# Performance work log

Measured on AMD Instinct MI355X. Metric: run time of the kernel, lower is better.

## Reference

```python
import jax, jax.numpy as jnp
import numpy as np

MEAN = jnp.array([0.485, 0.456, 0.406], dtype=jnp.float32).reshape(3, 1, 1)
STD = jnp.array([0.229, 0.224, 0.225], dtype=jnp.float32).reshape(3, 1, 1)
BLOCK = 8  # JPEG DCT block size


def _conv2(x, k):
    # x: [B,H,W], k: [kh,kw] -> SAME conv per image
    kern = k[None, None].astype(x.dtype)
    y = jax.lax.conv_general_dilated(x[:, None], kern, (1, 1), 'SAME')
    return y[:, 0]


def _box3(x):
    return _conv2(x, jnp.ones((3, 3), jnp.float32) / 9.0)


def _normalize(f):
    # per-image min-max to [0,1]; zero map if degenerate (matches _normalize)
    fmin = f.min(axis=(-2, -1), keepdims=True)
    fmax = f.max(axis=(-2, -1), keepdims=True)
    rng = fmax - fmin
    safe = jnp.where(rng < 1e-8, 1.0, rng)
    return jnp.where(rng < 1e-8, 0.0, (f - fmin) / safe)


def _forward(x):
    # denormalize ImageNet stats, clamp, scale to [0,255] (continuous; uint8 round omitted)
    img = jnp.clip(x * STD + MEAN, 0.0, 1.0) * 255.0  # [B,3,H,W]
    gray = 0.299 * img[:, 0] + 0.587 * img[:, 1] + 0.114 * img[:, 2]  # [B,H,W]

    # --- channel 0: spectral residual anomaly (FFT) ---
    F = jnp.fft.fft2(gray)
    logmag = jnp.log(jnp.abs(F) + 1e-8)
    resid = logmag - _box3(logmag)            # high-freq log-spectrum residual
    phase = jnp.angle(F)
    sal = jnp.abs(jnp.fft.ifft2(jnp.exp(resid) * jnp.exp(1j * phase))) ** 2
    M_spec = _normalize(sal)

    # --- channel 1: resampling artifact (2nd-derivative / Laplacian magnitude) ---
    lap_k = jnp.array([[0., 1., 0.], [1., -4., 1.], [0., 1., 0.]], jnp.float32)
    M_resamp = _normalize(jnp.abs(_conv2(gray, lap_k)))

    # --- channel 2: JPEG blockiness (gradient energy on 8x8 block boundaries) ---
    B, H, W = gray.shape
    dh = jnp.abs(gray - jnp.roll(gray, 1, axis=-1))  # horizontal neighbor diff
    dv = jnp.abs(gray - jnp.roll(gray, 1, axis=-2))  # vertical neighbor diff
    col_mask = (jnp.arange(W) % BLOCK == 0).astype(gray.dtype)  # [W]
    row_mask = (jnp.arange(H) % BLOCK == 0).astype(gray.dtype)  # [H]
    blockiness = dh * col_mask[None, None, :] + dv * row_mask[None, :, None]
    M_jpeg = _normalize(blockiness)

    return jnp.stack([M_spec, M_resamp, M_jpeg], axis=1)  # [B,3,H,W]


def setup_inputs() -> dict:
    key = jax.random.key(0)
    x = jax.random.normal(key, (16, 3, 512, 512), dtype=jnp.float32)
    return {"x": x}


def reference(x):
    return _forward(x)
```

## Files before the change

kernel.cpp:

```cpp
#include <hip/hip_runtime.h>
#include <hip/hip_bf16.h>
#include <math.h>

#define W 512
#define H 512
#define HW 262144
#define NB 16

__device__ __forceinline__ int brev9(int x) { return (int)(__brev((unsigned)x) >> 23); }
__device__ __forceinline__ int pad17(int i) { return i + (i >> 4); }

__device__ __forceinline__ void block_minmax_atomic(float vmin, float vmax,
                                                    unsigned* minU, unsigned* maxU) {
  #pragma unroll
  for (int o = 32; o; o >>= 1) {
    vmin = fminf(vmin, __shfl_xor(vmin, o));
    vmax = fmaxf(vmax, __shfl_xor(vmax, o));
  }
  __shared__ float smin[4], smax[4];
  int wid = threadIdx.x >> 6;
  int lane = threadIdx.x & 63;
  if (lane == 0) { smin[wid] = vmin; smax[wid] = vmax; }
  __syncthreads();
  if (threadIdx.x == 0) {
    int nw = (blockDim.x + 63) >> 6;
    float m = smin[0], M = smax[0];
    for (int i = 1; i < nw; ++i) { m = fminf(m, smin[i]); M = fmaxf(M, smax[i]); }
    atomicMin(minU, __float_as_uint(m));
    atomicMax(maxU, __float_as_uint(M));
  }
  __syncthreads();
}

__global__ void k_init(unsigned* mm) {
  int t = threadIdx.x;
  if (t < 48) mm[t] = 0x7F800000u;
  else if (t < 96) mm[t] = 0u;
}

__device__ __forceinline__ float gray_one(float r, float g, float b) {
  float R = fminf(fmaxf(fmaf(r, 0.229f, 0.485f), 0.f), 1.f) * 255.f;
  float G = fminf(fmaxf(fmaf(g, 0.224f, 0.456f), 0.f), 1.f) * 255.f;
  float B = fminf(fmaxf(fmaf(b, 0.225f, 0.406f), 0.f), 1.f) * 255.f;
  return fmaf(0.299f, R, fmaf(0.587f, G, 0.114f * B));
}

__device__ __forceinline__ void tw_init(float2* tw, int t, int nthr) {
  for (int k = t; k < 256; k += nthr) {
    float sn, cs;
    __sincosf(-6.283185307179586f * (float)k * (1.f / 512.f), &sn, &cs);
    tw[k] = make_float2(cs, sn);
  }
}

#define QUAD_BODY(LOADA0, LOADA1, LOADA2, LOADA3)                                   \
  float e0r = sre[LOADA0], e0i = sim[LOADA0];                                       \
  float e1r = sre[LOADA1], e1i = sim[LOADA1];                                       \
  float e2r = sre[LOADA2], e2i = sim[LOADA2];                                       \
  float e3r = sre[LOADA3], e3i = sim[LOADA3];                                       \
  float t1r = fmaf(e1r, w1c, -e1i * w1s), t1i = fmaf(e1r, w1s, e1i * w1c);          \
  float t3r = fmaf(e3r, w1c, -e3i * w1s), t3i = fmaf(e3r, w1s, e3i * w1c);          \
  float A0r = e0r + t1r, A0i = e0i + t1i;                                           \
  float A1r = e0r - t1r, A1i = e0i - t1i;                                           \
  float A2r = e2r + t3r, A2i = e2i + t3i;                                           \
  float A3r = e2r - t3r, A3i = e2i - t3i;                                           \
  float t2r = fmaf(A2r, w2c, -A2i * w2s), t2i = fmaf(A2r, w2s, A2i * w2c);          \
  float t4r = fmaf(A3r, w3c, -A3i * w3s), t4i = fmaf(A3r, w3s, A3i * w3c);          \
  sre[LOADA0] = A0r + t2r; sim[LOADA0] = A0i + t2i;                                 \
  sre[LOADA2] = A0r - t2r; sim[LOADA2] = A0i - t2i;                                 \
  sre[LOADA1] = A1r + t4r; sim[LOADA1] = A1i + t4i;                                 \
  sre[LOADA3] = A1r - t4r; sim[LOADA3] = A1i - t4i;

template <int DIR>
__device__ __forceinline__ void fft512_q(float* sre, float* sim, const float2* tw, int t) {
  #pragma unroll
  for (int sp = 1; sp <= 7; sp += 2) {
    __syncthreads();
    int h = 1 << (sp - 1);
    int j = t & (h - 1);
    int q = ((t >> (sp - 1)) << (sp + 1)) + j;
    float2 w1t = tw[j << (9 - sp)];
    float2 w2t = tw[j << (8 - sp)];
    float2 w3t = tw[(j + h) << (8 - sp)];
    float w1c = w1t.x, w1s = (DIR > 0) ? w1t.y : -w1t.y;
    float w2c = w2t.x, w2s = (DIR > 0) ? w2t.y : -w2t.y;
    float w3c = w3t.x, w3s = (DIR > 0) ? w3t.y : -w3t.y;
    int a0 = pad17(q), a1 = pad17(q + h), a2 = pad17(q + 2 * h), a3 = pad17(q + 3 * h);
    QUAD_BODY(a0, a1, a2, a3)
  }
  __syncthreads();
  #pragma unroll
  for (int bb = 0; bb < 2; ++bb) {
    int bf = t + (bb << 7);
    float2 w = tw[bf];
    float cs = w.x, sn = (DIR > 0) ? w.y : -w.y;
    int a0 = pad17(bf), a1 = pad17(bf + 256);
    float ur = sre[a0], ui = sim[a0];
    float vr = sre[a1], vi = sim[a1];
    float tr = fmaf(vr, cs, -vi * sn);
    float ti = fmaf(vr, sn, vi * cs);
    sre[a0] = ur + tr; sim[a0] = ui + ti;
    sre[a1] = ur - tr; sim[a1] = ui - ti;
  }
  __syncthreads();
}

template <int DIR>
__device__ __forceinline__ void fft512x8_q(float* sre, float* sim, const float2* tw,
                                           int c, int tc) {
  #pragma unroll
  for (int sp = 1; sp <= 7; sp += 2) {
    __syncthreads();
    int h = 1 << (sp - 1);
    #pragma unroll
    for (int m = 0; m < 4; ++m) {
      int qq = tc + (m << 5);
      int j = qq & (h - 1);
      int q = ((qq >> (sp - 1)) << (sp + 1)) + j;
      float2 w1t = tw[j << (9 - sp)];
      float2 w2t = tw[j << (8 - sp)];
      float2 w3t = tw[(j + h) << (8 - sp)];
      float w1c = w1t.x, w1s = (DIR > 0) ? w1t.y : -w1t.y;
      float w2c = w2t.x, w2s = (DIR > 0) ? w2t.y : -w2t.y;
      float w3c = w3t.x, w3s = (DIR > 0) ? w3t.y : -w3t.y;
      int a0 = q * 9 + c, a1 = (q + h) * 9 + c, a2 = (q + 2 * h) * 9 + c, a3 = (q + 3 * h) * 9 + c;
      QUAD_BODY(a0, a1, a2, a3)
    }
  }
  __syncthreads();
  #pragma unroll
  for (int bb = 0; bb < 8; ++bb) {
    int bf = tc + (bb << 5);
    float2 w = tw[bf];
    float cs = w.x, sn = (DIR > 0) ? w.y : -w.y;
    int a0 = bf * 9 + c, a1 = (bf + 256) * 9 + c;
    float ur = sre[a0], ui = sim[a0];
    float vr = sre[a1], vi = sim[a1];
    float tr = fmaf(vr, cs, -vi * sn);
    float ti = fmaf(vr, sn, vi * cs);
    sre[a0] = ur + tr; sim[a0] = ui + ti;
    sre[a1] = ur - tr; sim[a1] = ui - ti;
  }
  __syncthreads();
}

__global__ void k_rowfft(const float* __restrict__ x, float* __restrict__ gray,
                         float2* __restrict__ C) {
  int r = blockIdx.x, b = blockIdx.y, t = threadIdx.x;
  __shared__ float sre[544], sim[544];
  __shared__ float2 tw[256];
  tw_init(tw, t, 128);
  const float* xr = x + (((size_t)(b * 3 + 0)) << 18) + r * W;
  const float* xg = x + (((size_t)(b * 3 + 1)) << 18) + r * W;
  const float* xb = x + (((size_t)(b * 3 + 2)) << 18) + r * W;
  float* gr = gray + (((size_t)b) << 18) + r * W;
  #pragma unroll
  for (int k = t; k < 512; k += 128) {
    float g = gray_one(xr[k], xg[k], xb[k]);
    gr[k] = g;
    int kr = pad17(brev9(k));
    sre[kr] = g; sim[kr] = 0.f;
  }
  fft512_q<1>(sre, sim, tw, t);
  float2* Crow = C + (((size_t)b) << 18) + r * W;
  #pragma unroll
  for (int k = t; k < 512; k += 128) {
    int kp = pad17(k);
    Crow[k] = make_float2(sre[kp], sim[kp]);
  }
}

__global__ void k_ch12(const float* __restrict__ gray, float* __restrict__ out, unsigned* mm) {
  int slab = blockIdx.x, b = blockIdx.y, t = threadIdx.x;
  const float* gb = gray + (((size_t)b) << 18);
  float* o1 = out + (((size_t)(b * 3 + 1)) << 18);
  float* o2 = out + (((size_t)(b * 3 + 2)) << 18);
  float mn1 = INFINITY, mx1 = -INFINITY, mn2 = INFINITY, mx2 = -INFINITY;
  for (int i4 = t; i4 < 32 * 128; i4 += 256) {
    int r = (slab << 5) + (i4 >> 7);
    int k4 = (i4 & 127) << 2;
    const float* row = gb + r * W;
    float4 c4 = *(const float4*)(row + k4);
    float s_lfw = row[(k4 + W - 1) & (W - 1)];
    float s_rt  = (k4 < W - 4) ? row[k4 + 4] : 0.f;
    float4 up4 = (r > 0)     ? *(const float4*)(gb + (r - 1) * W + k4) : make_float4(0.f, 0.f, 0.f, 0.f);
    float4 dn4 = (r < H - 1) ? *(const float4*)(gb + (r + 1) * W + k4) : make_float4(0.f, 0.f, 0.f, 0.f);
    float c[4]  = {c4.x, c4.y, c4.z, c4.w};
    float up[4] = {up4.x, up4.y, up4.z, up4.w};
    float dn[4] = {dn4.x, dn4.y, dn4.z, dn4.w};
    float lap[4], blk[4];
    #pragma unroll
    for (int e = 0; e < 4; ++e) {
      float lf = (e == 0) ? ((k4 > 0) ? s_lfw : 0.f) : c[e - 1];
      float rt = (e == 3) ? s_rt : c[e + 1];
      lap[e] = fabsf(lf + rt + up[e] + dn[e] - 4.f * c[e]);
      mn1 = fminf(mn1, lap[e]); mx1 = fmaxf(mx1, lap[e]);
    }
    bool rowb = ((r & 7) == 0);
    float pv[4] = {0.f, 0.f, 0.f, 0.f};
    if (rowb) {
      int rp = (r + H - 1) & (H - 1);
      float4 p4 = *(const float4*)(gb + rp * W + k4);
      pv[0] = p4.x; pv[1] = p4.y; pv[2] = p4.z; pv[3] = p4.w;
    }
    #pragma unroll
    for (int e = 0; e < 4; ++e) {
      float v = 0.f;
      if (e == 0 && ((k4 & 7) == 0)) v += fabsf(c[0] - s_lfw);
      if (rowb) v += fabsf(c[e] - pv[e]);
      blk[e] = v;
      mn2 = fminf(mn2, v); mx2 = fmaxf(mx2, v);
    }
    *(float4*)(o1 + r * W + k4) = make_float4(lap[0], lap[1], lap[2], lap[3]);
    *(float4*)(o2 + r * W + k4) = make_float4(blk[0], blk[1], blk[2], blk[3]);
  }
  block_minmax_atomic(mn1, mx1, mm + (b * 3 + 1), mm + 48 + (b * 3 + 1));
  block_minmax_atomic(mn2, mx2, mm + (b * 3 + 2), mm + 48 + (b * 3 + 2));
}

__global__ void k_colfft_fwd(float2* __restrict__ C, float* __restrict__ L) {
  int b = blockIdx.y, col0 = blockIdx.x << 3, t = threadIdx.x;
  __shared__ float sre[512 * 9], sim[512 * 9];
  __shared__ float2 tw[256];
  tw_init(tw, t, 256);
  float2* Cb = C + (((size_t)b) << 18);
  int c = t & 7, q = t >> 3;
  #pragma unroll
  for (int it = 0; it < 16; ++it) {
    int r = (it << 5) + q;
    float2 v = Cb[r * W + col0 + c];
    int rr = brev9(r);
    sre[rr * 9 + c] = v.x; sim[rr * 9 + c] = v.y;
  }
  fft512x8_q<1>(sre, sim, tw, t >> 5, t & 31);
  float* Lb = L + (((size_t)b) << 18);
  #pragma unroll
  for (int it = 0; it < 16; ++it) {
    int r = (it << 5) + q;
    float re = sre[r * 9 + c], im = sim[r * 9 + c];
    Cb[r * W + col0 + c] = make_float2(re, im);
    Lb[r * W + col0 + c] = logf(sqrtf(fmaf(re, re, im * im)) + 1e-8f);
  }
}

__global__ void k_rowifft_g(float2* __restrict__ C, const float* __restrict__ L) {
  int r = blockIdx.x, b = blockIdx.y, t = threadIdx.x;
  __shared__ float sre[544], sim[544], l0[512], lm[512], lp[512];
  __shared__ float2 tw[256];
  tw_init(tw, t, 128);
  const float* Lb = L + (((size_t)b) << 18);
  #pragma unroll
  for (int k = t; k < 512; k += 128) {
    l0[k] = Lb[r * W + k];
    lm[k] = (r > 0) ? Lb[(r - 1) * W + k] : 0.f;
    lp[k] = (r < H - 1) ? Lb[(r + 1) * W + k] : 0.f;
  }
  __syncthreads();
  float2* Crow = C + (((size_t)b) << 18) + r * W;
  #pragma unroll
  for (int k = t; k < 512; k += 128) {
    float sum = lm[k] + l0[k] + lp[k];
    if (k > 0)     sum += lm[k - 1] + l0[k - 1] + lp[k - 1];
    if (k < W - 1) sum += lm[k + 1] + l0[k + 1] + lp[k + 1];
    float resid = l0[k] - sum * (1.f / 9.f);
    float2 cv = Crow[k];
    float mag = sqrtf(fmaf(cv.x, cv.x, cv.y * cv.y));
    float er = __expf(resid);
    float gr, gi;
    if (mag > 1e-30f) { float tt = er / mag; gr = cv.x * tt; gi = cv.y * tt; }
    else { gr = er; gi = 0.f; }
    int kr = pad17(brev9(k));
    sre[kr] = gr; sim[kr] = gi;
  }
  fft512_q<-1>(sre, sim, tw, t);
  #pragma unroll
  for (int k = t; k < 512; k += 128) {
    int kp = pad17(k);
    Crow[k] = make_float2(sre[kp] * (1.f / 512.f), sim[kp] * (1.f / 512.f));
  }
}

__global__ void k_colifft_sal(const float2* __restrict__ C, float* __restrict__ out, unsigned* mm) {
  int b = blockIdx.y, col0 = blockIdx.x << 3, t = threadIdx.x;
  __shared__ float sre[512 * 9], sim[512 * 9];
  __shared__ float2 tw[256];
  tw_init(tw, t, 256);
  const float2* Cb = C + (((size_t)b) << 18);
  int c = t & 7, q = t >> 3;
  #pragma unroll
  for (int it = 0; it < 16; ++it) {
    int r = (it << 5) + q;
    float2 v = Cb[r * W + col0 + c];
    int rr = brev9(r);
    sre[rr * 9 + c] = v.x; sim[rr * 9 + c] = v.y;
  }
  fft512x8_q<-1>(sre, sim, tw, t >> 5, t & 31);
  float* ob = out + (((size_t)(b * 3 + 0)) << 18);
  float mn = INFINITY, mx = -INFINITY;
  #pragma unroll
  for (int it = 0; it < 16; ++it) {
    int r = (it << 5) + q;
    float re = sre[r * 9 + c], im = sim[r * 9 + c];
    float sal = fmaf(re, re, im * im) * 3.814697265625e-6f;
    ob[r * W + col0 + c] = sal;
    mn = fminf(mn, sal); mx = fmaxf(mx, sal);
  }
  block_minmax_atomic(mn, mx, mm + b * 3, mm + 48 + b * 3);
}

__global__ void k_norm(float* __restrict__ out, const unsigned* __restrict__ mm) {
  int i = blockIdx.x * blockDim.x + threadIdx.x;
  size_t base = ((size_t)i) << 2;
  int map = (int)(base >> 18);
  float mn = __uint_as_float(mm[map]);
  float mx = __uint_as_float(mm[48 + map]);
  float rng = mx - mn;
  float4 v = *(float4*)(out + base);
  float4 o;
  if (rng < 1e-8f) {
    o = make_float4(0.f, 0.f, 0.f, 0.f);
  } else {
    float inv = 1.f / rng;
    o.x = (v.x - mn) * inv;
    o.y = (v.y - mn) * inv;
    o.z = (v.z - mn) * inv;
    o.w = (v.w - mn) * inv;
  }
  *(float4*)(out + base) = o;
}

extern "C" void kernel_launch(void* const* d_in, const int* in_sizes, int n_in,
                              void* d_out, int out_size, void* d_ws, size_t ws_size,
                              hipStream_t stream) {
  const float* x = (const float*)d_in[0];
  float* out = (float*)d_out;

  float* gray = (float*)d_ws;
  float2* C = (float2*)((char*)d_ws + (size_t)NB * HW * sizeof(float));
  float* L = (float*)((char*)C + (size_t)NB * HW * sizeof(float2));
  unsigned* mm = (unsigned*)((char*)L + (size_t)NB * HW * sizeof(float));

  k_init<<<1, 96, 0, stream>>>(mm);
  k_rowfft<<<dim3(H, NB), 128, 0, stream>>>(x, gray, C);
  k_ch12<<<dim3(16, NB), 256, 0, stream>>>(gray, out, mm);
  k_colfft_fwd<<<dim3(W / 8, NB), 256, 0, stream>>>(C, L);
  k_rowifft_g<<<dim3(H, NB), 128, 0, stream>>>(C, L);
  k_colifft_sal<<<dim3(W / 8, NB), 256, 0, stream>>>(C, out, mm);
  k_norm<<<12288, 256, 0, stream>>>(out, mm);
}
```

Before: 226.7 us.

## Fuse pipeline into one persistent cooperative kernel with grid syncs

Replaces the seven-kernel launch sequence with one persistent cooperative kernel that runs every stage in turn, separated by grid-wide syncs: row FFT, Laplacian/blockiness maps, column FFT with log-magnitude, row inverse FFT, column inverse FFT with saliency, then min/max reduction and normalization. Per-block atomic min/max is replaced by per-slab partial min/max arrays reduced in a dedicated stage, and the ch1/ch2 work now runs in smaller 8-row slabs interleaved with the column FFT phase. The aim is to remove launch gaps and the init kernel. The cost is several grid barriers, and occupancy is limited by the shared-memory footprint and launch_bounds. If the cooperative launch fails, it falls back to the old launches.

New measurement: 548.4 us. 2.42x slower.

```diff
diff --git a/kernel.cpp b/kernel.cpp
--- a/kernel.cpp
+++ b/kernel.cpp
@@ -1,56 +1,23 @@
 #include <hip/hip_runtime.h>
-#include <hip/hip_bf16.h>
+#include <hip/hip_cooperative_groups.h>
 #include <math.h>
+
+namespace cg = cooperative_groups;
 
 #define W 512
 #define H 512
 #define HW 262144
 #define NB 16
+#define TPB 256
 
 __device__ __forceinline__ int brev9(int x) { return (int)(__brev((unsigned)x) >> 23); }
 __device__ __forceinline__ int pad17(int i) { return i + (i >> 4); }
-
-__device__ __forceinline__ void block_minmax_atomic(float vmin, float vmax,
-                                                    unsigned* minU, unsigned* maxU) {
-  #pragma unroll
-  for (int o = 32; o; o >>= 1) {
-    vmin = fminf(vmin, __shfl_xor(vmin, o));
-    vmax = fmaxf(vmax, __shfl_xor(vmax, o));
-  }
-  __shared__ float smin[4], smax[4];
-  int wid = threadIdx.x >> 6;
-  int lane = threadIdx.x & 63;
-  if (lane == 0) { smin[wid] = vmin; smax[wid] = vmax; }
-  __syncthreads();
-  if (threadIdx.x == 0) {
-    int nw = (blockDim.x + 63) >> 6;
-    float m = smin[0], M = smax[0];
-    for (int i = 1; i < nw; ++i) { m = fminf(m, smin[i]); M = fmaxf(M, smax[i]); }
-    atomicMin(minU, __float_as_uint(m));
-    atomicMax(maxU, __float_as_uint(M));
-  }
-  __syncthreads();
-}
-
-__global__ void k_init(unsigned* mm) {
-  int t = threadIdx.x;
-  if (t < 48) mm[t] = 0x7F800000u;
-  else if (t < 96) mm[t] = 0u;
-}
 
 __device__ __forceinline__ float gray_one(float r, float g, float b) {
   float R = fminf(fmaxf(fmaf(r, 0.229f, 0.485f), 0.f), 1.f) * 255.f;
   float G = fminf(fmaxf(fmaf(g, 0.224f, 0.456f), 0.f), 1.f) * 255.f;
   float B = fminf(fmaxf(fmaf(b, 0.225f, 0.406f), 0.f), 1.f) * 255.f;
   return fmaf(0.299f, R, fmaf(0.587f, G, 0.114f * B));
-}
-
-__device__ __forceinline__ void tw_init(float2* tw, int t, int nthr) {
-  for (int k = t; k < 256; k += nthr) {
-    float sn, cs;
-    __sincosf(-6.283185307179586f * (float)k * (1.f / 512.f), &sn, &cs);
-    tw[k] = make_float2(cs, sn);
-  }
 }
 
 #define QUAD_BODY(LOADA0, LOADA1, LOADA2, LOADA3)                                   \
@@ -142,6 +109,288 @@
     sre[a1] = ur - tr; sim[a1] = ui - ti;
   }
   __syncthreads();
+}
+
+
+__device__ __forceinline__ void block_minmax_store(float vmin, float vmax,
+                                                   float* dmn, float* dmx,
+                                                   float* s_mn, float* s_mx) {
+  #pragma unroll
+  for (int o = 32; o; o >>= 1) {
+    vmin = fminf(vmin, __shfl_xor(vmin, o));
+    vmax = fmaxf(vmax, __shfl_xor(vmax, o));
+  }
+  int wid = threadIdx.x >> 6, lane = threadIdx.x & 63;
+  if (lane == 0) { s_mn[wid] = vmin; s_mx[wid] = vmax; }
+  __syncthreads();
+  if (threadIdx.x == 0) {
+    *dmn = fminf(fminf(s_mn[0], s_mn[1]), fminf(s_mn[2], s_mn[3]));
+    *dmx = fmaxf(fmaxf(s_mx[0], s_mx[1]), fmaxf(s_mx[2], s_mx[3]));
+  }
+  __syncthreads();
+}
+
+__global__ __launch_bounds__(TPB, 4) void k_mega(
+    const float* __restrict__ x, float* gray, float2* C, float* L,
+    float* mm, float* pmn, float* pmx, float* out) {
+  cg::grid_group gg = cg::this_grid();
+  __shared__ float smem[9216];
+  __shared__ float2 tw[256];
+  __shared__ float s_mn[4], s_mx[4];
+  const int g = blockIdx.x, t = threadIdx.x, nblk = gridDim.x;
+
+  {
+    float sn, cs;
+    __sincosf(-6.283185307179586f * (float)t * (1.f / 512.f), &sn, &cs);
+    tw[t] = make_float2(cs, sn);
+  }
+
+  {
+    const int sub = t >> 7, tt = t & 127;
+    float* sre = smem + sub * 1088;
+    float* sim = sre + 544;
+    for (int p = g; p < 4096; p += nblk) {
+      int R = (p << 1) + sub;
+      int b = R >> 9, r = R & 511;
+      const float* xr = x + (((size_t)(b * 3 + 0)) << 18) + r * W;
+      const float* xg = x + (((size_t)(b * 3 + 1)) << 18) + r * W;
+      const float* xb = x + (((size_t)(b * 3 + 2)) << 18) + r * W;
+      float* gr = gray + (((size_t)b) << 18) + r * W;
+      #pragma unroll
+      for (int k = tt; k < 512; k += 128) {
+        float gv = gray_one(xr[k], xg[k], xb[k]);
+        gr[k] = gv;
+        int kr = pad17(brev9(k));
+        sre[kr] = gv; sim[kr] = 0.f;
+      }
+      fft512_q<1>(sre, sim, tw, tt);
+      float2* Crow = C + (((size_t)b) << 18) + r * W;
+      #pragma unroll
+      for (int k = tt; k < 512; k += 128) {
+        int kp = pad17(k);
+        Crow[k] = make_float2(sre[kp], sim[kp]);
+      }
+      __syncthreads();
+    }
+  }
+  gg.sync();
+
+  for (int u2 = g; u2 < 1024; u2 += nblk) {
+    const int b = u2 >> 6, slab = u2 & 63, r0 = slab << 3;
+    const float* gb = gray + (((size_t)b) << 18);
+    float* o1 = out + (((size_t)(b * 3 + 1)) << 18);
+    float* o2 = out + (((size_t)(b * 3 + 2)) << 18);
+    float mn1 = INFINITY, mx1 = -INFINITY, mn2 = INFINITY, mx2 = -INFINITY;
+    for (int u = t; u < 8 * 128; u += TPB) {
+      int r = r0 + (u >> 7);
+      int k4 = (u & 127) << 2;
+      const float* row = gb + r * W;
+      float4 c4 = *(const float4*)(row + k4);
+      float s_lfw = row[(k4 + W - 1) & (W - 1)];
+      float s_rt  = (k4 < W - 4) ? row[k4 + 4] : 0.f;
+      float4 up4 = (r > 0)     ? *(const float4*)(gb + (r - 1) * W + k4) : make_float4(0.f, 0.f, 0.f, 0.f);
+      float4 dn4 = (r < H - 1) ? *(const float4*)(gb + (r + 1) * W + k4) : make_float4(0.f, 0.f, 0.f, 0.f);
+      float c[4]  = {c4.x, c4.y, c4.z, c4.w};
+      float up[4] = {up4.x, up4.y, up4.z, up4.w};
+      float dn[4] = {dn4.x, dn4.y, dn4.z, dn4.w};
+      float lap[4], blk[4];
+      #pragma unroll
+      for (int e = 0; e < 4; ++e) {
+        float lf = (e == 0) ? ((k4 > 0) ? s_lfw : 0.f) : c[e - 1];
+        float rt = (e == 3) ? s_rt : c[e + 1];
+        lap[e] = fabsf(lf + rt + up[e] + dn[e] - 4.f * c[e]);
+        mn1 = fminf(mn1, lap[e]); mx1 = fmaxf(mx1, lap[e]);
+      }
+      bool rowb = ((r & 7) == 0);
+      float pv[4] = {0.f, 0.f, 0.f, 0.f};
+      if (rowb) {
+        int rp = (r + H - 1) & (H - 1);
+        float4 p4 = *(const float4*)(gb + rp * W + k4);
+        pv[0] = p4.x; pv[1] = p4.y; pv[2] = p4.z; pv[3] = p4.w;
+      }
+      #pragma unroll
+      for (int e = 0; e < 4; ++e) {
+        float v = 0.f;
+        if (e == 0 && ((k4 & 7) == 0)) v += fabsf(c[0] - s_lfw);
+        if (rowb) v += fabsf(c[e] - pv[e]);
+        blk[e] = v;
+        mn2 = fminf(mn2, v); mx2 = fmaxf(mx2, v);
+      }
+      *(float4*)(o1 + r * W + k4) = make_float4(lap[0], lap[1], lap[2], lap[3]);
+      *(float4*)(o2 + r * W + k4) = make_float4(blk[0], blk[1], blk[2], blk[3]);
+    }
+    block_minmax_store(mn1, mx1, &pmn[(b * 3 + 1) * 64 + slab], &pmx[(b * 3 + 1) * 64 + slab], s_mn, s_mx);
+    block_minmax_store(mn2, mx2, &pmn[(b * 3 + 2) * 64 + slab], &pmx[(b * 3 + 2) * 64 + slab], s_mn, s_mx);
+  }
+
+  for (int u2 = g; u2 < 1024; u2 += nblk) {
+    const int b = u2 >> 6, col0 = (u2 & 63) << 3;
+    float* sre = smem;
+    float* sim = smem + 4608;
+    float2* Cb = C + (((size_t)b) << 18);
+    int c = t & 7, q = t >> 3;
+    __syncthreads();
+    #pragma unroll
+    for (int it = 0; it < 16; ++it) {
+      int r = (it << 5) + q;
+      float2 v = Cb[r * W + col0 + c];
+      int rr = brev9(r);
+      sre[rr * 9 + c] = v.x; sim[rr * 9 + c] = v.y;
+    }
+    fft512x8_q<1>(sre, sim, tw, t >> 5, t & 31);
+    float* Lb = L + (((size_t)b) << 18);
+    #pragma unroll
+    for (int it = 0; it < 16; ++it) {
+      int r = (it << 5) + q;
+      float re = sre[r * 9 + c], im = sim[r * 9 + c];
+      Cb[r * W + col0 + c] = make_float2(re, im);
+      Lb[r * W + col0 + c] = logf(sqrtf(fmaf(re, re, im * im)) + 1e-8f);
+    }
+  }
+  gg.sync();
+
+  {
+    const int sub = t >> 7, tt = t & 127;
+    float* sre = smem + sub * 1088;
+    float* sim = sre + 544;
+    float* l0 = smem + 2176 + sub * 1536;
+    float* lm = l0 + 512;
+    float* lp = l0 + 1024;
+    for (int p = g; p < 4096; p += nblk) {
+      int R = (p << 1) + sub;
+      int b = R >> 9, r = R & 511;
+      const float* Lb = L + (((size_t)b) << 18);
+      #pragma unroll
+      for (int k = tt; k < 512; k += 128) {
+        l0[k] = Lb[r * W + k];
+        lm[k] = (r > 0) ? Lb[(r - 1) * W + k] : 0.f;
+        lp[k] = (r < H - 1) ? Lb[(r + 1) * W + k] : 0.f;
+      }
+      __syncthreads();
+      float2* Crow = C + (((size_t)b) << 18) + r * W;
+      #pragma unroll
+      for (int k = tt; k < 512; k += 128) {
+        float sum = lm[k] + l0[k] + lp[k];
+        if (k > 0)     sum += lm[k - 1] + l0[k - 1] + lp[k - 1];
+        if (k < W - 1) sum += lm[k + 1] + l0[k + 1] + lp[k + 1];
+        float resid = l0[k] - sum * (1.f / 9.f);
+        float2 cv = Crow[k];
+        float mag = sqrtf(fmaf(cv.x, cv.x, cv.y * cv.y));
+        float er = __expf(resid);
+        float gr2, gi;
+        if (mag > 1e-30f) { float tt2 = er / mag; gr2 = cv.x * tt2; gi = cv.y * tt2; }
+        else { gr2 = er; gi = 0.f; }
+        int kr = pad17(brev9(k));
+        sre[kr] = gr2; sim[kr] = gi;
+      }
+      fft512_q<-1>(sre, sim, tw, tt);
+      #pragma unroll
+      for (int k = tt; k < 512; k += 128) {
+        int kp = pad17(k);
+        Crow[k] = make_float2(sre[kp] * (1.f / 512.f), sim[kp] * (1.f / 512.f));
+      }
+      __syncthreads();
+    }
+  }
+  gg.sync();
+
+  for (int u2 = g; u2 < 1024; u2 += nblk) {
+    const int b = u2 >> 6, slab = u2 & 63, col0 = slab << 3;
+    float* sre = smem;
+    float* sim = smem + 4608;
+    const float2* Cb = C + (((size_t)b) << 18);
+    int c = t & 7, q = t >> 3;
+    __syncthreads();
+    #pragma unroll
+    for (int it = 0; it < 16; ++it) {
+      int r = (it << 5) + q;
+      float2 v = Cb[r * W + col0 + c];
+      int rr = brev9(r);
+      sre[rr * 9 + c] = v.x; sim[rr * 9 + c] = v.y;
+    }
+    fft512x8_q<-1>(sre, sim, tw, t >> 5, t & 31);
+    float* ob = out + (((size_t)(b * 3 + 0)) << 18);
+    float mn = INFINITY, mx = -INFINITY;
+    #pragma unroll
+    for (int it = 0; it < 16; ++it) {
+      int r = (it << 5) + q;
+      float re = sre[r * 9 + c], im = sim[r * 9 + c];
+      float sal = fmaf(re, re, im * im) * 3.814697265625e-6f;
+      ob[r * W + col0 + c] = sal;
+      mn = fminf(mn, sal); mx = fmaxf(mx, sal);
+    }
+    block_minmax_store(mn, mx, &pmn[(b * 3 + 0) * 64 + slab], &pmx[(b * 3 + 0) * 64 + slab], s_mn, s_mx);
+  }
+  gg.sync();
+
+  for (int m = g; m < 48; m += nblk) {
+    if (t < 64) {
+      float vmn = pmn[m * 64 + t];
+      float vmx = pmx[m * 64 + t];
+      #pragma unroll
+      for (int o = 32; o; o >>= 1) {
+        vmn = fminf(vmn, __shfl_xor(vmn, o));
+        vmx = fmaxf(vmx, __shfl_xor(vmx, o));
+      }
+      if (t == 0) { mm[m] = vmn; mm[48 + m] = vmx; }
+    }
+  }
+  gg.sync();
+
+  for (int idx = g * TPB + t; idx < 3145728; idx += nblk * TPB) {
+    int map = idx >> 16;
+    float mn = mm[map], mx = mm[48 + map];
+    float rng = mx - mn;
+    float4 v = *(float4*)(out + ((size_t)idx << 2));
+    float4 o;
+    if (rng < 1e-8f) {
+      o = make_float4(0.f, 0.f, 0.f, 0.f);
+    } else {
+      float inv = 1.f / rng;
+      o.x = (v.x - mn) * inv;
+      o.y = (v.y - mn) * inv;
+      o.z = (v.z - mn) * inv;
+      o.w = (v.w - mn) * inv;
+    }
+    *(float4*)(out + ((size_t)idx << 2)) = o;
+  }
+}
+
+
+__device__ __forceinline__ void block_minmax_atomic(float vmin, float vmax,
+                                                    unsigned* minU, unsigned* maxU) {
+  #pragma unroll
+  for (int o = 32; o; o >>= 1) {
+    vmin = fminf(vmin, __shfl_xor(vmin, o));
+    vmax = fmaxf(vmax, __shfl_xor(vmax, o));
+  }
+  __shared__ float smin[4], smax[4];
+  int wid = threadIdx.x >> 6;
+  int lane = threadIdx.x & 63;
+  if (lane == 0) { smin[wid] = vmin; smax[wid] = vmax; }
+  __syncthreads();
+  if (threadIdx.x == 0) {
+    int nw = (blockDim.x + 63) >> 6;
+    float m = smin[0], M = smax[0];
+    for (int i = 1; i < nw; ++i) { m = fminf(m, smin[i]); M = fmaxf(M, smax[i]); }
+    atomicMin(minU, __float_as_uint(m));
+    atomicMax(maxU, __float_as_uint(M));
+  }
+  __syncthreads();
+}
+
+__global__ void k_init(unsigned* mm) {
+  int t = threadIdx.x;
+  if (t < 48) mm[t] = 0x7F800000u;
+  else if (t < 96) mm[t] = 0u;
+}
+
+__device__ __forceinline__ void tw_init(float2* tw, int t, int nthr) {
+  for (int k = t; k < 256; k += nthr) {
+    float sn, cs;
+    __sincosf(-6.283185307179586f * (float)k * (1.f / 512.f), &sn, &cs);
+    tw[k] = make_float2(cs, sn);
+  }
 }
 
 __global__ void k_rowfft(const float* __restrict__ x, float* __restrict__ gray,
@@ -338,13 +587,35 @@
   float* gray = (float*)d_ws;
   float2* C = (float2*)((char*)d_ws + (size_t)NB * HW * sizeof(float));
   float* L = (float*)((char*)C + (size_t)NB * HW * sizeof(float2));
-  unsigned* mm = (unsigned*)((char*)L + (size_t)NB * HW * sizeof(float));
-
-  k_init<<<1, 96, 0, stream>>>(mm);
-  k_rowfft<<<dim3(H, NB), 128, 0, stream>>>(x, gray, C);
-  k_ch12<<<dim3(16, NB), 256, 0, stream>>>(gray, out, mm);
-  k_colfft_fwd<<<dim3(W / 8, NB), 256, 0, stream>>>(C, L);
-  k_rowifft_g<<<dim3(H, NB), 128, 0, stream>>>(C, L);
-  k_colifft_sal<<<dim3(W / 8, NB), 256, 0, stream>>>(C, out, mm);
-  k_norm<<<12288, 256, 0, stream>>>(out, mm);
-}
+  void* mmv = (void*)((char*)L + (size_t)NB * HW * sizeof(float));
+
+  bool done = false;
+  int occ = 0;
+  hipError_t qe = hipOccupancyMaxActiveBlocksPerMultiprocessor(&occ, k_mega, TPB, 0);
+  if (qe == hipSuccess && occ > 0) {
+    int nblk = occ * 256;
+    if (nblk > 2048) nblk = 2048;
+    float* mmf = (float*)mmv;
+    float* pmn = mmf + 96;
+    float* pmx = pmn + 48 * 64;
+    void* args[] = {(void*)&x, (void*)&gray, (void*)&C, (void*)&L,
+                    (void*)&mmf, (void*)&pmn, (void*)&pmx, (void*)&out};
+    hipError_t le = hipLaunchCooperativeKernel((const void*)k_mega, dim3(nblk),
+                                               dim3(TPB), args, 0, stream);
+    if (le == hipSuccess) done = true;
+    else (void)hipGetLastError();
+  } else {
+    (void)hipGetLastError();
+  }
+
+  if (!done) {
+    unsigned* mmu = (unsigned*)mmv;
+    k_init<<<1, 96, 0, stream>>>(mmu);
+    k_rowfft<<<dim3(H, NB), 128, 0, stream>>>(x, gray, C);
+    k_ch12<<<dim3(16, NB), 256, 0, stream>>>(gray, out, mmu);
+    k_colfft_fwd<<<dim3(W / 8, NB), 256, 0, stream>>>(C, L);
+    k_rowifft_g<<<dim3(H, NB), 128, 0, stream>>>(C, L);
+    k_colifft_sal<<<dim3(W / 8, NB), 256, 0, stream>>>(C, out, mmu);
+    k_norm<<<12288, 256, 0, stream>>>(out, mmu);
+  }
+}
```
